# Performance work log

Hardware: AMD Instinct MI355X
Metric: run time of the kernel (lower is better)

The kernel has to match this reference:

```python
import jax, jax.numpy as jnp
import numpy as np

N_NODES = 100000
N_EDGES = 1600000
FEATURE_DIM, CONDITION_DIM, HIDDEN_DIM, LATENT_DIM = 256, 64, 128, 64


def setup_inputs() -> dict:
    key = jax.random.key(0)
    ks = jax.random.split(key, 12)

    def glorot(k, fan_in, fan_out):
        s = np.sqrt(6.0 / (fan_in + fan_out)).astype(np.float32)
        return jax.random.uniform(k, (fan_in, fan_out), jnp.float32, -s, s)

    return {
        "feature": jax.random.normal(ks[0], (N_NODES, FEATURE_DIM), jnp.float32),
        "condition": jax.random.normal(ks[1], (N_NODES, CONDITION_DIM), jnp.float32),
        "edge_index": jax.random.randint(ks[2], (2, N_EDGES), 0, N_NODES, jnp.int64),
        "W_f2h": glorot(ks[3], FEATURE_DIM, HIDDEN_DIM),
        "b_f2h": jnp.zeros((HIDDEN_DIM,), jnp.float32),
        "W_c2h": glorot(ks[4], CONDITION_DIM, HIDDEN_DIM),
        "b_c2h": jnp.zeros((HIDDEN_DIM,), jnp.float32),
        "W_h2h": glorot(ks[5], 2 * HIDDEN_DIM, HIDDEN_DIM),
        "b_h2h": jnp.zeros((HIDDEN_DIM,), jnp.float32),
        "W_h2l": glorot(ks[6], HIDDEN_DIM, LATENT_DIM),
        "b_h2l": jnp.zeros((LATENT_DIM,), jnp.float32),
    }


def reference(feature, condition, edge_index, W_f2h, b_f2h, W_c2h, b_c2h,
              W_h2h, b_h2h, W_h2l, b_h2l):
    N = feature.shape[0]
    self_loops = jnp.arange(N, dtype=edge_index.dtype)
    src = jnp.concatenate([edge_index[0], self_loops])  # message sources (j)
    dst = jnp.concatenate([edge_index[1], self_loops])  # message targets (i)

    # symmetric GCN normalization: D^{-1/2} (A+I) D^{-1/2}
    deg = jax.ops.segment_sum(jnp.ones(dst.shape[0], feature.dtype), dst,
                              num_segments=N)
    dinv = jnp.where(deg > 0, jax.lax.rsqrt(deg), 0.0)
    norm = dinv[src] * dinv[dst]  # [E+N]

    def gcn_conv(x, W, b):
        xl = x @ W                                   # [N, out]
        msg = xl[src] * norm[:, None]                # gather + scale
        return jax.ops.segment_sum(msg, dst, num_segments=N) + b

    f2h = jnp.tanh(gcn_conv(feature, W_f2h, b_f2h))
    c2h = jnp.tanh(gcn_conv(condition, W_c2h, b_c2h))
    h = jnp.concatenate([f2h, c2h], axis=1)          # [N, 2*hidden]
    h = jnp.tanh(gcn_conv(h, W_h2h, b_h2h))
    z = gcn_conv(h, W_h2l, b_h2l)
    return z
```

## Files before the change

### kernel.cpp

```cpp
#include <hip/hip_runtime.h>
#include <cmath>
#include <cstdint>


typedef _Float16 f16;
typedef _Float16 f16x8 __attribute__((ext_vector_type(8)));
typedef _Float16 f16x4 __attribute__((ext_vector_type(4)));
typedef float f32x4 __attribute__((ext_vector_type(4)));
typedef unsigned int u32x4 __attribute__((ext_vector_type(4)));
typedef unsigned int u32x2 __attribute__((ext_vector_type(2)));

__global__ void count_zero_kernel(int* __restrict__ count, int N) {
    int i = blockIdx.x * 256 + threadIdx.x;
    if (i < N) count[i] = 0;
}

__global__ void count_rank_kernel(const int* __restrict__ dst, int* __restrict__ count,
                                  int* __restrict__ rank, int E) {
    int e = blockIdx.x * 256 + threadIdx.x;
    if (e < E) rank[e] = atomicAdd(&count[dst[e]], 1);
}

__global__ void dinv_kernel(const int* __restrict__ count, float* __restrict__ dinv, int N) {
    int i = blockIdx.x * 256 + threadIdx.x;
    if (i < N) dinv[i] = rsqrtf((float)(count[i] + 1));
}

constexpr int SCAN_VPT = 8;
constexpr int SCAN_TILE = 256 * SCAN_VPT;

__global__ __launch_bounds__(256) void scan_partial_kernel(const int* __restrict__ count,
                                                           int* __restrict__ blocksums, int N) {
    __shared__ int red[256];
    const int t = threadIdx.x;
    int base = blockIdx.x * SCAN_TILE + t * SCAN_VPT;
    int s = 0;
#pragma unroll
    for (int i = 0; i < SCAN_VPT; ++i) {
        int idx = base + i;
        if (idx < N) s += count[idx];
    }
    red[t] = s;
    __syncthreads();
    for (int off = 128; off > 0; off >>= 1) {
        if (t < off) red[t] += red[t + off];
        __syncthreads();
    }
    if (t == 0) blocksums[blockIdx.x] = red[0];
}

__global__ __launch_bounds__(1024) void scan_blocksums_kernel(int* __restrict__ blocksums, int nb) {
    __shared__ int sh[1024];
    const int t = threadIdx.x;
    int v = (t < nb) ? blocksums[t] : 0;
    sh[t] = v;
    __syncthreads();
    for (int off = 1; off < 1024; off <<= 1) {
        int u = (t >= off) ? sh[t - off] : 0;
        __syncthreads();
        sh[t] += u;
        __syncthreads();
    }
    if (t < nb) blocksums[t] = sh[t] - v;
}

__global__ __launch_bounds__(256) void scan_final_kernel(const int* __restrict__ count,
                                                         const int* __restrict__ blocksums,
                                                         int* __restrict__ row_ptr, int N) {
    __shared__ int red[256];
    const int t = threadIdx.x;
    int base = blockIdx.x * SCAN_TILE + t * SCAN_VPT;
    int vals[SCAN_VPT];
    int s = 0;
#pragma unroll
    for (int i = 0; i < SCAN_VPT; ++i) {
        int idx = base + i;
        vals[i] = (idx < N) ? count[idx] : 0;
        s += vals[i];
    }
    red[t] = s;
    __syncthreads();
    for (int off = 1; off < 256; off <<= 1) {
        int u = (t >= off) ? red[t - off] : 0;
        __syncthreads();
        red[t] += u;
        __syncthreads();
    }
    int run = red[t] - s + blocksums[blockIdx.x];
#pragma unroll
    for (int i = 0; i < SCAN_VPT; ++i) {
        int idx = base + i;
        if (idx < N) {
            row_ptr[idx] = run;
            run += vals[i];
            if (idx == N - 1) row_ptr[N] = run;
        }
    }
}

__global__ void fill_kernel(const int* __restrict__ src, const int* __restrict__ dst,
                            const int* __restrict__ rank, const float* __restrict__ dinv,
                            const int* __restrict__ row_ptr, long long* __restrict__ csr, int E) {
    int e = blockIdx.x * 256 + threadIdx.x;
    if (e >= E) return;
    int s = src[e];
    int d = dst[e];
    int pos = row_ptr[d] + rank[e];
    float nrm = dinv[s] * dinv[d];
    long long v = ((long long)(unsigned)__float_as_int(nrm) << 32) | (unsigned)s;
    __builtin_nontemporal_store(v, csr + pos);
}

__global__ void wprep_kernel(const float* __restrict__ W, f16* __restrict__ wt_hi,
                             f16* __restrict__ wt_lo, int K, int M) {
    int idx = blockIdx.x * 256 + threadIdx.x;
    if (idx >= K * M) return;
    int k = idx / M, m = idx % M;
    float w = W[idx];
    f16 h = (f16)w;
    wt_hi[(size_t)m * K + k] = h;
    wt_lo[(size_t)m * K + k] = (f16)(w - (float)h);
}

__global__ void cond_to_xl_kernel(const float* __restrict__ x, f16* __restrict__ XL, int N) {
    int i = blockIdx.x * 256 + threadIdx.x;
    if (i >= N * 16) return;
    int node = i >> 4, q = i & 15;
    float4 v = ((const float4*)x)[i];
    union { f16 h[4]; uint2 u; } p;
    p.h[0] = (f16)v.x; p.h[1] = (f16)v.y; p.h[2] = (f16)v.z; p.h[3] = (f16)v.w;
    *(uint2*)(XL + (size_t)node * 192 + 128 + q * 4) = p.u;
}

template <int K, int M, bool BIAS_TANH, bool X_IS_HALF>
__global__ __launch_bounds__(256) void gemm_mfma_kernel(
    const void* __restrict__ Xv, const f16* __restrict__ Wth,
    const f16* __restrict__ Wtl, const float* __restrict__ bias,
    f16* __restrict__ out, int ld, int colOff, int ldx, int N) {
    constexpr int BM = 128, BK = 32, XP = 40;
    constexpr int SW = M / 4;
    constexpr int CT = SW / 16;
    constexpr int RT = BM / 16;
    __shared__ f16 xs[BM * XP];
    __shared__ f16 whs[M * XP];
    __shared__ f16 wls[M * XP];

    const int tid = threadIdx.x;
    const int lane = tid & 63;
    const int wv = tid >> 6;
    const int m16 = lane & 15;
    const int quad = lane >> 4;
    const int row0 = blockIdx.x * BM;

    f32x4 acc[RT][CT];
#pragma unroll
    for (int rt = 0; rt < RT; ++rt)
#pragma unroll
        for (int ct = 0; ct < CT; ++ct) acc[rt][ct] = (f32x4){0.f, 0.f, 0.f, 0.f};

    for (int k0 = 0; k0 < K; k0 += BK) {
        if (X_IS_HALF) {
            const f16* X = (const f16*)Xv;
#pragma unroll
            for (int i = 0; i < 2; ++i) {
                int c = i * 256 + tid;
                int r = c >> 2, ko = (c & 3) * 8;
                uint4 v = make_uint4(0u, 0u, 0u, 0u);
                if (row0 + r < N) v = *(const uint4*)(X + (size_t)(row0 + r) * ldx + k0 + ko);
                *(uint4*)(&xs[r * XP + ko]) = v;
            }
        } else {
            const float* X = (const float*)Xv;
#pragma unroll
            for (int i = 0; i < 4; ++i) {
                int c = i * 256 + tid;
                int r = c >> 3, kq = (c & 7) * 4;
                float4 v = make_float4(0.f, 0.f, 0.f, 0.f);
                if (row0 + r < N) v = *(const float4*)(X + (size_t)(row0 + r) * ldx + k0 + kq);
                union { f16 h[4]; uint2 u; } p;
                p.h[0] = (f16)v.x; p.h[1] = (f16)v.y; p.h[2] = (f16)v.z; p.h[3] = (f16)v.w;
                *(uint2*)(&xs[r * XP + kq]) = p.u;
            }
        }
#pragma unroll
        for (int i = 0; i < (M * 4) / 256; ++i) {
            int c = i * 256 + tid;
            int n = c >> 2, ko = (c & 3) * 8;
            *(uint4*)(&whs[n * XP + ko]) = *(const uint4*)(Wth + (size_t)n * K + k0 + ko);
            *(uint4*)(&wls[n * XP + ko]) = *(const uint4*)(Wtl + (size_t)n * K + k0 + ko);
        }
        __syncthreads();

        f16x8 bh[CT], bl[CT];
#pragma unroll
        for (int ct = 0; ct < CT; ++ct) {
            bh[ct] = *(const f16x8*)(&whs[(wv * SW + ct * 16 + m16) * XP + quad * 8]);
            bl[ct] = *(const f16x8*)(&wls[(wv * SW + ct * 16 + m16) * XP + quad * 8]);
        }
#pragma unroll
        for (int rt = 0; rt < RT; ++rt) {
            f16x8 a = *(const f16x8*)(&xs[(rt * 16 + m16) * XP + quad * 8]);
#pragma unroll
            for (int ct = 0; ct < CT; ++ct) {
                acc[rt][ct] = __builtin_amdgcn_mfma_f32_16x16x32_f16(a, bh[ct], acc[rt][ct], 0, 0, 0);
                acc[rt][ct] = __builtin_amdgcn_mfma_f32_16x16x32_f16(a, bl[ct], acc[rt][ct], 0, 0, 0);
            }
        }
        __syncthreads();
    }

    float brs[CT];
    if (BIAS_TANH) {
#pragma unroll
        for (int ct = 0; ct < CT; ++ct) brs[ct] = bias[wv * SW + ct * 16 + m16];
    }

#pragma unroll
    for (int rt = 0; rt < RT; ++rt) {
#pragma unroll
        for (int r = 0; r < 4; ++r) {
            int row = row0 + rt * 16 + quad * 4 + r;
            if (row < N) {
                f16* op = out + (size_t)row * ld + colOff + wv * SW + m16;
#pragma unroll
                for (int ct = 0; ct < CT; ++ct) {
                    float v = acc[rt][ct][r];
                    if (BIAS_TANH) v = tanhf(v + brs[ct]);
                    op[ct * 16] = (f16)v;
                }
            }
        }
    }
}

template <int M, bool TANH, bool HAS_BIAS, bool OUT_F32>
__global__ __launch_bounds__(256) void gather_h_kernel(
    const f16* __restrict__ xl, const float* __restrict__ b,
    const float* __restrict__ dinv, const int* __restrict__ row_ptr,
    const long long* __restrict__ csr, void* __restrict__ outv,
    int ld, int colOff, int N) {
    constexpr int TPN = M / 8;
    int gid = blockIdx.x * 256 + threadIdx.x;
    int node = gid / TPN;
    int t = gid % TPN;
    if (node >= N) return;

    float di = dinv[node];
    float self = di * di;
    f16x8 x = *(const f16x8*)(xl + (size_t)node * M + t * 8);
    float acc[8];
#pragma unroll
    for (int j = 0; j < 8; ++j) acc[j] = (float)x[j] * self;
    if (HAS_BIAS) {
        float4 b0 = *(const float4*)(b + t * 8);
        float4 b1 = *(const float4*)(b + t * 8 + 4);
        acc[0] += b0.x; acc[1] += b0.y; acc[2] += b0.z; acc[3] += b0.w;
        acc[4] += b1.x; acc[5] += b1.y; acc[6] += b1.z; acc[7] += b1.w;
    }

    int p = row_ptr[node];
    const int p1 = row_ptr[node + 1];
    const int last = p1 - 1;
    long long e0 = 0, e1 = 0, e2 = 0, e3 = 0;
    if (p < p1) {
        e0 = __builtin_nontemporal_load(csr + p);
        e1 = __builtin_nontemporal_load(csr + (p + 1 < p1 ? p + 1 : last));
        e2 = __builtin_nontemporal_load(csr + (p + 2 < p1 ? p + 2 : last));
        e3 = __builtin_nontemporal_load(csr + (p + 3 < p1 ? p + 3 : last));
    }
    while (p < p1) {
        const long long c0 = e0, c1 = e1, c2 = e2, c3 = e3;
        const int pn = p + 4;
        if (pn < p1) {
            e0 = __builtin_nontemporal_load(csr + pn);
            e1 = __builtin_nontemporal_load(csr + (pn + 1 < p1 ? pn + 1 : last));
            e2 = __builtin_nontemporal_load(csr + (pn + 2 < p1 ? pn + 2 : last));
            e3 = __builtin_nontemporal_load(csr + (pn + 3 < p1 ? pn + 3 : last));
        }
        int s0 = (int)c0, s1 = (int)c1, s2 = (int)c2, s3 = (int)c3;
        float n0 = __int_as_float((int)(c0 >> 32));
        float n1 = (p + 1 < p1) ? __int_as_float((int)(c1 >> 32)) : 0.f;
        float n2 = (p + 2 < p1) ? __int_as_float((int)(c2 >> 32)) : 0.f;
        float n3 = (p + 3 < p1) ? __int_as_float((int)(c3 >> 32)) : 0.f;
        f16x8 v0 = *(const f16x8*)(xl + (size_t)s0 * M + t * 8);
        f16x8 v1 = *(const f16x8*)(xl + (size_t)s1 * M + t * 8);
        f16x8 v2 = *(const f16x8*)(xl + (size_t)s2 * M + t * 8);
        f16x8 v3 = *(const f16x8*)(xl + (size_t)s3 * M + t * 8);
#pragma unroll
        for (int j = 0; j < 8; ++j)
            acc[j] += ((float)v0[j] * n0 + (float)v1[j] * n1) +
                      ((float)v2[j] * n2 + (float)v3[j] * n3);
        p = pn;
    }

    if (TANH) {
#pragma unroll
        for (int j = 0; j < 8; ++j) acc[j] = tanhf(acc[j]);
    }

    if (OUT_F32) {
        float* op = (float*)outv + (size_t)node * ld + colOff + t * 8;
        f32x4 o0 = {acc[0], acc[1], acc[2], acc[3]};
        f32x4 o1 = {acc[4], acc[5], acc[6], acc[7]};
        __builtin_nontemporal_store(o0, (f32x4*)op);
        __builtin_nontemporal_store(o1, (f32x4*)(op + 4));
    } else {
        union { f16 h[8]; u32x4 u; } o;
#pragma unroll
        for (int j = 0; j < 8; ++j) o.h[j] = (f16)acc[j];
        __builtin_nontemporal_store(o.u, (u32x4*)((f16*)outv + (size_t)node * ld + colOff + t * 8));
    }
}

__global__ __launch_bounds__(256) void gather_fused_kernel(
    const f16* __restrict__ XL, const float* __restrict__ bA,
    const float* __restrict__ dinv, const int* __restrict__ row_ptr,
    const long long* __restrict__ csr, f16* __restrict__ out, int N) {
    int gid = blockIdx.x * 256 + threadIdx.x;
    int node = gid >> 4;
    int t = gid & 15;
    if (node >= N) return;

    float di = dinv[node];
    float self = di * di;
    const f16* base = XL + (size_t)node * 192;
    f16x8 xa = *(const f16x8*)(base + t * 8);
    f16x4 xc = *(const f16x4*)(base + 128 + t * 4);
    float accA[8], accC[4];
#pragma unroll
    for (int j = 0; j < 8; ++j) accA[j] = (float)xa[j] * self;
#pragma unroll
    for (int j = 0; j < 4; ++j) accC[j] = (float)xc[j] * self;
    {
        float4 b0 = *(const float4*)(bA + t * 8);
        float4 b1 = *(const float4*)(bA + t * 8 + 4);
        accA[0] += b0.x; accA[1] += b0.y; accA[2] += b0.z; accA[3] += b0.w;
        accA[4] += b1.x; accA[5] += b1.y; accA[6] += b1.z; accA[7] += b1.w;
    }

    int p = row_ptr[node];
    const int p1 = row_ptr[node + 1];
    const int last = p1 - 1;
    long long e0 = 0, e1 = 0, e2 = 0, e3 = 0;
    if (p < p1) {
        e0 = __builtin_nontemporal_load(csr + p);
        e1 = __builtin_nontemporal_load(csr + (p + 1 < p1 ? p + 1 : last));
        e2 = __builtin_nontemporal_load(csr + (p + 2 < p1 ? p + 2 : last));
        e3 = __builtin_nontemporal_load(csr + (p + 3 < p1 ? p + 3 : last));
    }
    while (p < p1) {
        const long long c0 = e0, c1 = e1, c2 = e2, c3 = e3;
        const int pn = p + 4;
        if (pn < p1) {
            e0 = __builtin_nontemporal_load(csr + pn);
            e1 = __builtin_nontemporal_load(csr + (pn + 1 < p1 ? pn + 1 : last));
            e2 = __builtin_nontemporal_load(csr + (pn + 2 < p1 ? pn + 2 : last));
            e3 = __builtin_nontemporal_load(csr + (pn + 3 < p1 ? pn + 3 : last));
        }
        int s0 = (int)c0, s1 = (int)c1, s2 = (int)c2, s3 = (int)c3;
        float n0 = __int_as_float((int)(c0 >> 32));
        float n1 = (p + 1 < p1) ? __int_as_float((int)(c1 >> 32)) : 0.f;
        float n2 = (p + 2 < p1) ? __int_as_float((int)(c2 >> 32)) : 0.f;
        float n3 = (p + 3 < p1) ? __int_as_float((int)(c3 >> 32)) : 0.f;
        const f16* r0 = XL + (size_t)s0 * 192;
        const f16* r1 = XL + (size_t)s1 * 192;
        const f16* r2 = XL + (size_t)s2 * 192;
        const f16* r3 = XL + (size_t)s3 * 192;
        f16x8 a0 = *(const f16x8*)(r0 + t * 8);
        f16x8 a1 = *(const f16x8*)(r1 + t * 8);
        f16x8 a2 = *(const f16x8*)(r2 + t * 8);
        f16x8 a3 = *(const f16x8*)(r3 + t * 8);
        f16x4 q0 = *(const f16x4*)(r0 + 128 + t * 4);
        f16x4 q1 = *(const f16x4*)(r1 + 128 + t * 4);
        f16x4 q2 = *(const f16x4*)(r2 + 128 + t * 4);
        f16x4 q3 = *(const f16x4*)(r3 + 128 + t * 4);
#pragma unroll
        for (int j = 0; j < 8; ++j)
            accA[j] += ((float)a0[j] * n0 + (float)a1[j] * n1) +
                       ((float)a2[j] * n2 + (float)a3[j] * n3);
#pragma unroll
        for (int j = 0; j < 4; ++j)
            accC[j] += ((float)q0[j] * n0 + (float)q1[j] * n1) +
                       ((float)q2[j] * n2 + (float)q3[j] * n3);
        p = pn;
    }

#pragma unroll
    for (int j = 0; j < 8; ++j) accA[j] = tanhf(accA[j]);

    union { f16 h[8]; u32x4 u; } oa;
#pragma unroll
    for (int j = 0; j < 8; ++j) oa.h[j] = (f16)accA[j];
    __builtin_nontemporal_store(oa.u, (u32x4*)(out + (size_t)node * 256 + t * 8));
    union { f16 h[4]; u32x2 u; } oc;
#pragma unroll
    for (int j = 0; j < 4; ++j) oc.h[j] = (f16)accC[j];
    __builtin_nontemporal_store(oc.u, (u32x2*)(out + (size_t)node * 256 + 128 + t * 4));
}

extern "C" void kernel_launch(void* const* d_in, const int* in_sizes, int n_in,
                              void* d_out, int out_size, void* d_ws, size_t ws_size,
                              hipStream_t stream) {
    const int FD = 256;

    const float* feature   = (const float*)d_in[0];
    const float* condition = (const float*)d_in[1];
    const int*   edge      = (const int*)d_in[2];
    const float* W_f2h = (const float*)d_in[3];
    const float* b_f2h = (const float*)d_in[4];
    const float* W_c2h = (const float*)d_in[5];
    const float* b_c2h = (const float*)d_in[6];
    const float* W_h2h = (const float*)d_in[7];
    const float* b_h2h = (const float*)d_in[8];
    const float* W_h2l = (const float*)d_in[9];
    const float* b_h2l = (const float*)d_in[10];
    float* out = (float*)d_out;

    const int N = in_sizes[0] / FD;
    const int E = in_sizes[2] / 2;
    const int* src = edge;
    const int* dst = edge + E;

    float* ws_f   = (float*)d_ws;
    float* dinv   = ws_f;
    int*   count  = (int*)(ws_f + N);
    int*   rowp   = count + N;
    int*   bsums  = rowp + N + 1;
    int*   rank   = bsums + 1024;
    long long* csr = (long long*)(((uintptr_t)(rank + E) + 15) & ~(uintptr_t)15);
    f16*   XL     = (f16*)(csr + E);
    f16*   B_h    = XL + (size_t)N * 192;
    f16*   wt1h   = B_h + (size_t)N * 256;
    f16*   wt1l   = wt1h + 128 * 256;
    f16*   wt2h   = wt1l + 128 * 256;
    f16*   wt2l   = wt2h + 128 * 64;
    f16*   wt3h   = wt2l + 128 * 64;
    f16*   wt3l   = wt3h + 128 * 256;
    f16*   wt4h   = wt3l + 128 * 256;
    f16*   wt4l   = wt4h + 64 * 128;

    const int TB = 256;
    dim3 blk(TB);
    const int nScanBlocks = (N + SCAN_TILE - 1) / SCAN_TILE;

    wprep_kernel<<<(256 * 128 + TB - 1) / TB, blk, 0, stream>>>(W_f2h, wt1h, wt1l, 256, 128);
    wprep_kernel<<<(64 * 128 + TB - 1) / TB, blk, 0, stream>>>(W_c2h, wt2h, wt2l, 64, 128);
    wprep_kernel<<<(256 * 128 + TB - 1) / TB, blk, 0, stream>>>(W_h2h, wt3h, wt3l, 256, 128);
    wprep_kernel<<<(128 * 64 + TB - 1) / TB, blk, 0, stream>>>(W_h2l, wt4h, wt4l, 128, 64);
    cond_to_xl_kernel<<<(N * 16 + TB - 1) / TB, blk, 0, stream>>>(condition, XL, N);

    count_zero_kernel<<<(N + TB - 1) / TB, blk, 0, stream>>>(count, N);
    count_rank_kernel<<<(E + TB - 1) / TB, blk, 0, stream>>>(dst, count, rank, E);
    dinv_kernel<<<(N + TB - 1) / TB, blk, 0, stream>>>(count, dinv, N);
    scan_partial_kernel<<<nScanBlocks, blk, 0, stream>>>(count, bsums, N);
    scan_blocksums_kernel<<<1, 1024, 0, stream>>>(bsums, nScanBlocks);
    scan_final_kernel<<<nScanBlocks, blk, 0, stream>>>(count, bsums, rowp, N);
    fill_kernel<<<(E + TB - 1) / TB, blk, 0, stream>>>(src, dst, rank, dinv, rowp, csr, E);

    const int gemm_grid = (N + 127) / 128;
    const int g128 = (N * 16 + TB - 1) / TB;
    const int g64  = (N * 8 + TB - 1) / TB;

    gemm_mfma_kernel<256, 128, false, false><<<gemm_grid, blk, 0, stream>>>(
        feature, wt1h, wt1l, nullptr, XL, 192, 0, 256, N);

    gather_fused_kernel<<<g128, blk, 0, stream>>>(
        XL, b_f2h, dinv, rowp, csr, B_h, N);

    gemm_mfma_kernel<64, 128, true, true><<<gemm_grid, blk, 0, stream>>>(
        (const void*)(B_h + 128), wt2h, wt2l, b_c2h, B_h, 256, 128, 256, N);

    gemm_mfma_kernel<256, 128, false, true><<<gemm_grid, blk, 0, stream>>>(
        B_h, wt3h, wt3l, nullptr, XL, 128, 0, 256, N);
    gather_h_kernel<128, true, true, false><<<g128, blk, 0, stream>>>(
        XL, b_h2h, dinv, rowp, csr, B_h, 128, 0, N);

    gemm_mfma_kernel<128, 64, false, true><<<gemm_grid, blk, 0, stream>>>(
        B_h, wt4h, wt4l, nullptr, XL, 64, 0, 128, N);
    gather_h_kernel<64, false, true, true><<<g64, blk, 0, stream>>>(
        XL, b_h2l, dinv, rowp, csr, out, 64, 0, N);
}
```

Baseline: 740.6 us.

## Pre-swizzle weights into MFMA fragment layout and drop LDS staging in GEMMs

Weights are now written by a single merged prep kernel in a fragment-major layout, so each lane loads its MFMA B operand straight from global memory. The GEMM drops its shared-memory staging and barriers and reads A rows directly from global. The dinv computation is folded into the partial scan, and the blocksum scan is folded into the final scan, which removes several small launches. The trade-off is that A loads become strided, uncoalesced 16-byte reads per lane with no cross-wave reuse, and the blocksum scan assumes at most 64 scan blocks.

```diff
diff --git a/kernel.cpp b/kernel.cpp
--- a/kernel.cpp
+++ b/kernel.cpp
@@ -21,15 +21,11 @@
     if (e < E) rank[e] = atomicAdd(&count[dst[e]], 1);
 }
 
-__global__ void dinv_kernel(const int* __restrict__ count, float* __restrict__ dinv, int N) {
-    int i = blockIdx.x * 256 + threadIdx.x;
-    if (i < N) dinv[i] = rsqrtf((float)(count[i] + 1));
-}
-
 constexpr int SCAN_VPT = 8;
 constexpr int SCAN_TILE = 256 * SCAN_VPT;
 
 __global__ __launch_bounds__(256) void scan_partial_kernel(const int* __restrict__ count,
+                                                           float* __restrict__ dinv,
                                                            int* __restrict__ blocksums, int N) {
     __shared__ int red[256];
     const int t = threadIdx.x;
@@ -38,7 +34,11 @@
 #pragma unroll
     for (int i = 0; i < SCAN_VPT; ++i) {
         int idx = base + i;
-        if (idx < N) s += count[idx];
+        if (idx < N) {
+            int c = count[idx];
+            dinv[idx] = rsqrtf((float)(c + 1));
+            s += c;
+        }
     }
     red[t] = s;
     __syncthreads();
@@ -49,26 +49,22 @@
     if (t == 0) blocksums[blockIdx.x] = red[0];
 }
 
-__global__ __launch_bounds__(1024) void scan_blocksums_kernel(int* __restrict__ blocksums, int nb) {
-    __shared__ int sh[1024];
-    const int t = threadIdx.x;
-    int v = (t < nb) ? blocksums[t] : 0;
-    sh[t] = v;
-    __syncthreads();
-    for (int off = 1; off < 1024; off <<= 1) {
-        int u = (t >= off) ? sh[t - off] : 0;
-        __syncthreads();
-        sh[t] += u;
-        __syncthreads();
-    }
-    if (t < nb) blocksums[t] = sh[t] - v;
-}
-
 __global__ __launch_bounds__(256) void scan_final_kernel(const int* __restrict__ count,
                                                          const int* __restrict__ blocksums,
-                                                         int* __restrict__ row_ptr, int N) {
+                                                         int* __restrict__ row_ptr, int N, int nb) {
     __shared__ int red[256];
+    __shared__ int bs[64];
     const int t = threadIdx.x;
+    if (t < 64) bs[t] = (t < nb) ? blocksums[t] : 0;
+    __syncthreads();
+    for (int off = 1; off < 64; off <<= 1) {
+        int u = (t < 64 && t >= off) ? bs[t - off] : 0;
+        __syncthreads();
+        if (t < 64) bs[t] += u;
+        __syncthreads();
+    }
+    const int myBase = (blockIdx.x > 0) ? bs[blockIdx.x - 1] : 0;
+
     int base = blockIdx.x * SCAN_TILE + t * SCAN_VPT;
     int vals[SCAN_VPT];
     int s = 0;
@@ -86,7 +82,7 @@
         red[t] += u;
         __syncthreads();
     }
-    int run = red[t] - s + blocksums[blockIdx.x];
+    int run = red[t] - s + myBase;
 #pragma unroll
     for (int i = 0; i < SCAN_VPT; ++i) {
         int idx = base + i;
@@ -111,15 +107,31 @@
     __builtin_nontemporal_store(v, csr + pos);
 }
 
-__global__ void wprep_kernel(const float* __restrict__ W, f16* __restrict__ wt_hi,
-                             f16* __restrict__ wt_lo, int K, int M) {
-    int idx = blockIdx.x * 256 + threadIdx.x;
-    if (idx >= K * M) return;
+__device__ inline void wprep_one(const float* __restrict__ W, f16* __restrict__ hi,
+                                 f16* __restrict__ lo, int M, int idx) {
     int k = idx / M, m = idx % M;
     float w = W[idx];
     f16 h = (f16)w;
-    wt_hi[(size_t)m * K + k] = h;
-    wt_lo[(size_t)m * K + k] = (f16)(w - (float)h);
+    int f = ((k >> 5) * (M >> 4) + (m >> 4)) * 512 + (((k >> 3) & 3) << 7) + ((m & 15) << 3) + (k & 7);
+    hi[f] = h;
+    lo[f] = (f16)(w - (float)h);
+}
+
+__global__ void wprep_all_kernel(const float* __restrict__ W1, f16* h1, f16* l1,
+                                 const float* __restrict__ W2, f16* h2, f16* l2,
+                                 const float* __restrict__ W3, f16* h3, f16* l3,
+                                 const float* __restrict__ W4, f16* h4, f16* l4) {
+    int b = blockIdx.x;
+    int t = threadIdx.x;
+    if (b < 128) {
+        wprep_one(W1, h1, l1, 128, b * 256 + t);
+    } else if (b < 160) {
+        wprep_one(W2, h2, l2, 128, (b - 128) * 256 + t);
+    } else if (b < 288) {
+        wprep_one(W3, h3, l3, 128, (b - 160) * 256 + t);
+    } else {
+        wprep_one(W4, h4, l4, 64, (b - 288) * 256 + t);
+    }
 }
 
 __global__ void cond_to_xl_kernel(const float* __restrict__ x, f16* __restrict__ XL, int N) {
@@ -133,17 +145,16 @@
 }
 
 template <int K, int M, bool BIAS_TANH, bool X_IS_HALF>
-__global__ __launch_bounds__(256) void gemm_mfma_kernel(
-    const void* __restrict__ Xv, const f16* __restrict__ Wth,
-    const f16* __restrict__ Wtl, const float* __restrict__ bias,
+__global__ __launch_bounds__(256) void gemm_direct_kernel(
+    const void* __restrict__ Xv, const f16* __restrict__ WFh,
+    const f16* __restrict__ WFl, const float* __restrict__ bias,
     f16* __restrict__ out, int ld, int colOff, int ldx, int N) {
-    constexpr int BM = 128, BK = 32, XP = 40;
+    constexpr int BM = 128;
     constexpr int SW = M / 4;
     constexpr int CT = SW / 16;
     constexpr int RT = BM / 16;
-    __shared__ f16 xs[BM * XP];
-    __shared__ f16 whs[M * XP];
-    __shared__ f16 wls[M * XP];
+    constexpr int KS = K / 32;
+    constexpr int MT = M / 16;
 
     const int tid = threadIdx.x;
     const int lane = tid & 63;
@@ -152,61 +163,46 @@
     const int quad = lane >> 4;
     const int row0 = blockIdx.x * BM;
 
+    int xr[RT];
+#pragma unroll
+    for (int rt = 0; rt < RT; ++rt) {
+        int r = row0 + rt * 16 + m16;
+        xr[rt] = r < N ? r : N - 1;
+    }
+
     f32x4 acc[RT][CT];
 #pragma unroll
     for (int rt = 0; rt < RT; ++rt)
 #pragma unroll
         for (int ct = 0; ct < CT; ++ct) acc[rt][ct] = (f32x4){0.f, 0.f, 0.f, 0.f};
 
-    for (int k0 = 0; k0 < K; k0 += BK) {
-        if (X_IS_HALF) {
-            const f16* X = (const f16*)Xv;
-#pragma unroll
-            for (int i = 0; i < 2; ++i) {
-                int c = i * 256 + tid;
-                int r = c >> 2, ko = (c & 3) * 8;
-                uint4 v = make_uint4(0u, 0u, 0u, 0u);
-                if (row0 + r < N) v = *(const uint4*)(X + (size_t)(row0 + r) * ldx + k0 + ko);
-                *(uint4*)(&xs[r * XP + ko]) = v;
+    for (int ks = 0; ks < KS; ++ks) {
+        const int k0 = ks * 32;
+        f16x8 bh[CT], bl[CT];
+#pragma unroll
+        for (int ct = 0; ct < CT; ++ct) {
+            const int fb = ((ks * MT + wv * CT + ct) << 9) + lane * 8;
+            bh[ct] = *(const f16x8*)(WFh + fb);
+            bl[ct] = *(const f16x8*)(WFl + fb);
+        }
+#pragma unroll
+        for (int rt = 0; rt < RT; ++rt) {
+            f16x8 a;
+            if (X_IS_HALF) {
+                a = *(const f16x8*)((const f16*)Xv + (size_t)xr[rt] * ldx + k0 + quad * 8);
+            } else {
+                const float* xp = (const float*)Xv + (size_t)xr[rt] * ldx + k0 + quad * 8;
+                f32x4 v0 = *(const f32x4*)xp;
+                f32x4 v1 = *(const f32x4*)(xp + 4);
+                a[0] = (f16)v0[0]; a[1] = (f16)v0[1]; a[2] = (f16)v0[2]; a[3] = (f16)v0[3];
+                a[4] = (f16)v1[0]; a[5] = (f16)v1[1]; a[6] = (f16)v1[2]; a[7] = (f16)v1[3];
             }
-        } else {
-            const float* X = (const float*)Xv;
-#pragma unroll
-            for (int i = 0; i < 4; ++i) {
-                int c = i * 256 + tid;
-                int r = c >> 3, kq = (c & 7) * 4;
-                float4 v = make_float4(0.f, 0.f, 0.f, 0.f);
-                if (row0 + r < N) v = *(const float4*)(X + (size_t)(row0 + r) * ldx + k0 + kq);
-                union { f16 h[4]; uint2 u; } p;
-                p.h[0] = (f16)v.x; p.h[1] = (f16)v.y; p.h[2] = (f16)v.z; p.h[3] = (f16)v.w;
-                *(uint2*)(&xs[r * XP + kq]) = p.u;
-            }
-        }
-#pragma unroll
-        for (int i = 0; i < (M * 4) / 256; ++i) {
-            int c = i * 256 + tid;
-            int n = c >> 2, ko = (c & 3) * 8;
-            *(uint4*)(&whs[n * XP + ko]) = *(const uint4*)(Wth + (size_t)n * K + k0 + ko);
-            *(uint4*)(&wls[n * XP + ko]) = *(const uint4*)(Wtl + (size_t)n * K + k0 + ko);
-        }
-        __syncthreads();
-
-        f16x8 bh[CT], bl[CT];
-#pragma unroll
-        for (int ct = 0; ct < CT; ++ct) {
-            bh[ct] = *(const f16x8*)(&whs[(wv * SW + ct * 16 + m16) * XP + quad * 8]);
-            bl[ct] = *(const f16x8*)(&wls[(wv * SW + ct * 16 + m16) * XP + quad * 8]);
-        }
-#pragma unroll
-        for (int rt = 0; rt < RT; ++rt) {
-            f16x8 a = *(const f16x8*)(&xs[(rt * 16 + m16) * XP + quad * 8]);
 #pragma unroll
             for (int ct = 0; ct < CT; ++ct) {
                 acc[rt][ct] = __builtin_amdgcn_mfma_f32_16x16x32_f16(a, bh[ct], acc[rt][ct], 0, 0, 0);
                 acc[rt][ct] = __builtin_amdgcn_mfma_f32_16x16x32_f16(a, bl[ct], acc[rt][ct], 0, 0, 0);
             }
         }
-        __syncthreads();
     }
 
     float brs[CT];
@@ -443,39 +439,35 @@
     dim3 blk(TB);
     const int nScanBlocks = (N + SCAN_TILE - 1) / SCAN_TILE;
 
-    wprep_kernel<<<(256 * 128 + TB - 1) / TB, blk, 0, stream>>>(W_f2h, wt1h, wt1l, 256, 128);
-    wprep_kernel<<<(64 * 128 + TB - 1) / TB, blk, 0, stream>>>(W_c2h, wt2h, wt2l, 64, 128);
-    wprep_kernel<<<(256 * 128 + TB - 1) / TB, blk, 0, stream>>>(W_h2h, wt3h, wt3l, 256, 128);
-    wprep_kernel<<<(128 * 64 + TB - 1) / TB, blk, 0, stream>>>(W_h2l, wt4h, wt4l, 128, 64);
+    wprep_all_kernel<<<320, blk, 0, stream>>>(W_f2h, wt1h, wt1l, W_c2h, wt2h, wt2l,
+                                              W_h2h, wt3h, wt3l, W_h2l, wt4h, wt4l);
     cond_to_xl_kernel<<<(N * 16 + TB - 1) / TB, blk, 0, stream>>>(condition, XL, N);
 
     count_zero_kernel<<<(N + TB - 1) / TB, blk, 0, stream>>>(count, N);
     count_rank_kernel<<<(E + TB - 1) / TB, blk, 0, stream>>>(dst, count, rank, E);
-    dinv_kernel<<<(N + TB - 1) / TB, blk, 0, stream>>>(count, dinv, N);
-    scan_partial_kernel<<<nScanBlocks, blk, 0, stream>>>(count, bsums, N);
-    scan_blocksums_kernel<<<1, 1024, 0, stream>>>(bsums, nScanBlocks);
-    scan_final_kernel<<<nScanBlocks, blk, 0, stream>>>(count, bsums, rowp, N);
+    scan_partial_kernel<<<nScanBlocks, blk, 0, stream>>>(count, dinv, bsums, N);
+    scan_final_kernel<<<nScanBlocks, blk, 0, stream>>>(count, bsums, rowp, N, nScanBlocks);
     fill_kernel<<<(E + TB - 1) / TB, blk, 0, stream>>>(src, dst, rank, dinv, rowp, csr, E);
 
     const int gemm_grid = (N + 127) / 128;
     const int g128 = (N * 16 + TB - 1) / TB;
     const int g64  = (N * 8 + TB - 1) / TB;
 
-    gemm_mfma_kernel<256, 128, false, false><<<gemm_grid, blk, 0, stream>>>(
+    gemm_direct_kernel<256, 128, false, false><<<gemm_grid, blk, 0, stream>>>(
         feature, wt1h, wt1l, nullptr, XL, 192, 0, 256, N);
 
     gather_fused_kernel<<<g128, blk, 0, stream>>>(
         XL, b_f2h, dinv, rowp, csr, B_h, N);
 
-    gemm_mfma_kernel<64, 128, true, true><<<gemm_grid, blk, 0, stream>>>(
+    gemm_direct_kernel<64, 128, true, true><<<gemm_grid, blk, 0, stream>>>(
         (const void*)(B_h + 128), wt2h, wt2l, b_c2h, B_h, 256, 128, 256, N);
 
-    gemm_mfma_kernel<256, 128, false, true><<<gemm_grid, blk, 0, stream>>>(
+    gemm_direct_kernel<256, 128, false, true><<<gemm_grid, blk, 0, stream>>>(
         B_h, wt3h, wt3l, nullptr, XL, 128, 0, 256, N);
     gather_h_kernel<128, true, true, false><<<g128, blk, 0, stream>>>(
         XL, b_h2h, dinv, rowp, csr, B_h, 128, 0, N);
 
-    gemm_mfma_kernel<128, 64, false, true><<<gemm_grid, blk, 0, stream>>>(
+    gemm_direct_kernel<128, 64, false, true><<<gemm_grid, blk, 0, stream>>>(
         B_h, wt4h, wt4l, nullptr, XL, 64, 0, 128, N);
     gather_h_kernel<64, false, true, true><<<g64, blk, 0, stream>>>(
         XL, b_h2l, dinv, rowp, csr, out, 64, 0, N);
```

New measurement: 750.1 us. About the same (+1.3%).
